# Kernel optimization log

Measured on AMD Instinct MI355X. Metric: run time of the kernel, lower is better.

The kernel has to match this reference:

```python
import jax, jax.numpy as jnp
import numpy as np

B, T, D, K = 16, 4096, 512, 128
ALPHA_MIN = 1e-06
OMEGA_MAX = float(np.pi)
SN_EPS = 1e-06


def setup_inputs() -> dict:
    key = jax.random.key(0)
    ks = jax.random.split(key, 7)
    x = jax.random.normal(ks[0], (B, T, D), jnp.float32)
    # irregular positive step sizes, mean ~ 1/T like the uniform-grid default
    dt = jax.random.uniform(ks[1], (B, T), jnp.float32, minval=0.1, maxval=1.9) * (1.0 / T)
    # replicate reset_parameters: target_alpha ~ U(0.01, 0.2), raw = log(expm1(alpha - alpha_min))
    target_alpha = jax.random.uniform(ks[2], (K,), jnp.float32, minval=0.01, maxval=0.2)
    s_real_raw = jnp.log(jnp.expm1(jnp.maximum(target_alpha - ALPHA_MIN, 1e-08)))
    s_imag = jax.random.uniform(ks[3], (K,), jnp.float32, minval=-np.pi, maxval=np.pi)
    # kaiming-uniform-ish proj weight [K, D] and bias [K]
    W = jax.random.normal(ks[4], (K, D), jnp.float32) * (1.0 / np.sqrt(D))
    bound = 1.0 / np.sqrt(D)
    bias = jax.random.uniform(ks[5], (K,), jnp.float32, minval=-bound, maxval=bound)
    b_log = jnp.zeros((K,), jnp.float32)  # torch stores [1,1,K]; broadcasting is identical
    u_sn = jax.random.normal(ks[6], (K,), jnp.float32)  # spectral-norm power-iteration vector
    return {"x": x, "dt": dt, "s_real_raw": s_real_raw, "s_imag": s_imag,
            "W": W, "bias": bias, "b_log": b_log, "u_sn": u_sn}


def _spectral_normalize(W, u):
    # one power iteration, u/v detached (as torch.nn.utils.spectral_norm does)
    v = W.T @ u
    v = v / (jnp.linalg.norm(v) + SN_EPS)
    u2 = W @ v
    u2 = u2 / (jnp.linalg.norm(u2) + SN_EPS)
    u2 = jax.lax.stop_gradient(u2)
    v = jax.lax.stop_gradient(v)
    sigma = u2 @ (W @ v)
    return W / sigma


def reference(x, dt, s_real_raw, s_imag, W, bias, b_log, u_sn):
    # x: [B,T,D], dt: [B,T] -> lap_feats [B,T,2K]
    alpha = jax.nn.softplus(s_real_raw) + ALPHA_MIN          # [K] strictly positive decay
    omega = jnp.clip(s_imag, -OMEGA_MAX, OMEGA_MAX)          # [K]
    Wsn = _spectral_normalize(W, u_sn)
    u = jnp.einsum('btd,kd->btk', x, Wsn) + bias             # spectral-norm projection
    dt3 = dt[..., None]                                      # [B,T,1]
    rho = jnp.exp(-alpha * dt3)                              # [B,T,K]
    theta = omega * dt3
    cos_t, sin_t = jnp.cos(theta), jnp.sin(theta)
    b_gain = jnp.exp(b_log)                                  # [K]
    inj = (1.0 - rho) * (b_gain * u)                         # [B,T,K]

    def step(carry, inp):
        c, s = carry
        r, ct, st, it = inp
        c_new = r * (c * ct - s * st) + it
        s_new = r * (c * st + s * ct) + it
        return (c_new, s_new), (c_new, s_new)

    seq = (jnp.moveaxis(rho, 1, 0), jnp.moveaxis(cos_t, 1, 0),
           jnp.moveaxis(sin_t, 1, 0), jnp.moveaxis(inj, 1, 0))  # each [T,B,K]
    init = (jnp.zeros((x.shape[0], K), x.dtype), jnp.zeros((x.shape[0], K), x.dtype))
    _, (C, S) = jax.lax.scan(step, init, seq)
    C = jnp.moveaxis(C, 0, 1)  # [B,T,K]
    S = jnp.moveaxis(S, 0, 1)
    return jnp.concatenate([C, S], axis=-1)
```

## Files before the change

### kernel.cpp

```cpp
#include <hip/hip_runtime.h>
#include <stdint.h>

#define BB 16
#define TT 4096
#define DDIM 512
#define KK 128
#define TCB 128
#define NCB (TT / TCB)
#define PI_F 3.14159265358979323846f

typedef unsigned short u16;
typedef __attribute__((ext_vector_type(8))) short short8;
typedef __attribute__((ext_vector_type(4))) float f32x4;

__device__ __forceinline__ uint32_t cvt_bf16_rn(float f) {
  uint32_t u = __float_as_uint(f);
  return (u + 0x7FFFu + ((u >> 16) & 1u)) >> 16;
}
__device__ __forceinline__ uint32_t pack2(float a, float b) {
  return cvt_bf16_rn(a) | (cvt_bf16_rn(b) << 16);
}
__device__ __forceinline__ void gload_lds16(const void* g, void* l) {
  __builtin_amdgcn_global_load_lds(
      (const __attribute__((address_space(1))) void*)g,
      (__attribute__((address_space(3))) void*)l, 16, 0, 0);
}

__global__ __launch_bounds__(256) void k_prep(
    const float* __restrict__ W, const float* __restrict__ u_sn,
    const float* __restrict__ s_real_raw, const float* __restrict__ s_imag,
    const float* __restrict__ bias, const float* __restrict__ b_log,
    const float* __restrict__ dt,
    float* __restrict__ params, u16* __restrict__ Wp, float* __restrict__ ct) {
  int gb = blockIdx.x;
  int tid = threadIdx.x;
  if (gb < 64) {
    int idx = gb * 256 + tid;
    int k = idx >> 7;
    int d = (idx & 127) * 4;
    float4 v = *(const float4*)&W[(size_t)k * DDIM + d];
    int tile = d >> 6, dl = d & 63;
    int slot = (dl >> 3) ^ (k & 7);
    int e = dl & 7;
    size_t base = (size_t)tile * 8192 + k * 64 + slot * 8 + e;
    uint2 p;
    p.x = pack2(v.x, v.y);
    p.y = pack2(v.z, v.w);
    *(uint2*)&Wp[base] = p;
  } else if (gb < 80) {
    __shared__ float sc[256];
    int b = gb - 64;
    const float* row = dt + (size_t)b * TT;
    float* orow = ct + (size_t)b * TT;
    float loc[16];
    float s = 0.f;
    int base = tid * 16;
    for (int i = 0; i < 16; ++i) { s += row[base + i]; loc[i] = s; }
    sc[tid] = s;
    __syncthreads();
    for (int off = 1; off < 256; off <<= 1) {
      float v = (tid >= off) ? sc[tid - off] : 0.f;
      __syncthreads();
      sc[tid] += v;
      __syncthreads();
    }
    float excl = sc[tid] - s;
    for (int i = 0; i < 16; ++i) orow[base + i] = excl + loc[i];
  } else {
    __shared__ float su[KK];
    __shared__ float sv[DDIM];
    __shared__ float red[4];
    __shared__ float wred[256];
    __shared__ float s_sig;
    if (tid < KK) su[tid] = u_sn[tid];
    __syncthreads();
    for (int rep = 0; rep < 2; ++rep) {
      int d = tid + rep * 256;
      float acc = 0.f;
      for (int k = 0; k < KK; ++k) acc += W[k * DDIM + d] * su[k];
      sv[d] = acc;
    }
    __syncthreads();
    float nn = 0.f;
    for (int rep = 0; rep < 2; ++rep) { float v = sv[tid + rep * 256]; nn += v * v; }
    for (int off = 32; off > 0; off >>= 1) nn += __shfl_down(nn, off, 64);
    if ((tid & 63) == 0) red[tid >> 6] = nn;
    __syncthreads();
    float vn2 = red[0] + red[1] + red[2] + red[3];
    __syncthreads();
    float vinv = 1.f / (sqrtf(vn2) + 1e-6f);
    for (int rep = 0; rep < 2; ++rep) sv[tid + rep * 256] *= vinv;
    __syncthreads();
    {
      int k = tid & 127, q = tid >> 7;
      const float* wrow = W + (size_t)k * DDIM + q * 256;
      float p = 0.f;
      for (int d = 0; d < 256; ++d) p += wrow[d] * sv[q * 256 + d];
      wred[tid] = p;
    }
    __syncthreads();
    float wv = 0.f;
    if (tid < KK) wv = wred[tid] + wred[tid + 128];
    float q = wv * wv;
    for (int off = 32; off > 0; off >>= 1) q += __shfl_down(q, off, 64);
    if ((tid & 63) == 0) red[tid >> 6] = q;
    __syncthreads();
    if (tid == 0) {
      float wn2 = red[0] + red[1] + red[2] + red[3];
      s_sig = wn2 / (sqrtf(wn2) + 1e-6f);
    }
    __syncthreads();
    if (tid < KK) {
      float inv_sigma = 1.f / s_sig;
      float sr = s_real_raw[tid];
      float alpha = ((sr > 20.f) ? sr : log1pf(expf(sr))) + 1e-6f;
      float om = fminf(fmaxf(s_imag[tid], -PI_F), PI_F);
      float bg = expf(b_log[tid]);
      params[tid] = alpha;
      params[KK + tid] = om;
      params[2 * KK + tid] = bg * inv_sigma;
      params[3 * KK + tid] = bg * bias[tid];
    }
  }
}

__global__ __launch_bounds__(512, 4) void k_gemm(
    const float* __restrict__ x, const u16* __restrict__ Wp,
    const float* __restrict__ dt, const float* __restrict__ ct,
    const float* __restrict__ params, u16* __restrict__ itvb,
    float* __restrict__ csum_re, float* __restrict__ csum_im) {
  __shared__ __align__(16) u16 smem[32768];

  const int chunk = blockIdx.x, b = blockIdx.y;
  const int tid = threadIdx.x;
  const int wv = tid >> 6, l = tid & 63;
  const int lm = l & 15, lg = l >> 4;
  const int kw = wv & 1, tw = wv >> 1;
  const int t0 = chunk * TCB;

  const int xr0 = tid >> 4;
  const int xc = (tid & 15) * 4;
  const size_t xbase = ((size_t)b * TT + t0 + xr0) * DDIM + xc;
  int xso[4];
#pragma unroll
  for (int q = 0; q < 4; ++q) {
    int row = xr0 + 32 * q;
    xso[q] = row * 64 + (((xc >> 3) ^ (row & 7)) << 3) + ((xc >> 2) & 1) * 4;
  }

  f32x4 acc[2][4];
#pragma unroll
  for (int m = 0; m < 2; ++m)
#pragma unroll
    for (int n = 0; n < 4; ++n) acc[m][n] = (f32x4)(0.0f);

  {
    const char* wsg = (const char*)Wp + (size_t)tid * 16;
    char* wd = (char*)smem + 32768 + tid * 16;
    gload_lds16(wsg, wd);
    gload_lds16(wsg + 8192, wd + 8192);
#pragma unroll
    for (int q = 0; q < 4; ++q) {
      float4 v = *(const float4*)(x + xbase + (size_t)(32 * q) * DDIM);
      uint2 p;
      p.x = pack2(v.x, v.y);
      p.y = pack2(v.z, v.w);
      *(uint2*)&smem[xso[q]] = p;
    }
  }
  __syncthreads();

  int cur = 0;
  for (int it = 0; it < 8; ++it) {
    float4 xf[4];
    if (it < 7) {
      const float* xp = x + xbase + (it + 1) * 64;
#pragma unroll
      for (int q = 0; q < 4; ++q)
        xf[q] = *(const float4*)(xp + (size_t)(32 * q) * DDIM);
      const char* wsg = (const char*)Wp + (size_t)(it + 1) * 16384 + tid * 16;
      char* wd = (char*)smem + 32768 + (cur ^ 1) * 16384 + tid * 16;
      gload_lds16(wsg, wd);
      gload_lds16(wsg + 8192, wd + 8192);
    }
    __builtin_amdgcn_sched_barrier(0);
    {
      const u16* xb = smem + cur * 8192;
      const u16* wb = smem + 16384 + cur * 8192;
      __builtin_amdgcn_s_setprio(1);
#pragma unroll
      for (int ks = 0; ks < 2; ++ks) {
        short8 fa[2], fb[4];
#pragma unroll
        for (int m = 0; m < 2; ++m) {
          int row = tw * 32 + m * 16 + lm;
          int sw = ((ks * 4 + lg) ^ (row & 7)) * 8;
          fa[m] = *(const short8*)&xb[row * 64 + sw];
        }
#pragma unroll
        for (int n = 0; n < 4; ++n) {
          int row = kw * 64 + n * 16 + lm;
          int sw = ((ks * 4 + lg) ^ (row & 7)) * 8;
          fb[n] = *(const short8*)&wb[row * 64 + sw];
        }
#pragma unroll
        for (int m = 0; m < 2; ++m)
#pragma unroll
          for (int n = 0; n < 4; ++n)
            acc[m][n] = __builtin_amdgcn_mfma_f32_16x16x32_bf16(fa[m], fb[n], acc[m][n], 0, 0, 0);
      }
      __builtin_amdgcn_s_setprio(0);
    }
    __builtin_amdgcn_sched_barrier(0);
    if (it < 7) {
      u16* xb = smem + (cur ^ 1) * 8192;
#pragma unroll
      for (int q = 0; q < 4; ++q) {
        uint2 p;
        p.x = pack2(xf[q].x, xf[q].y);
        p.y = pack2(xf[q].z, xf[q].w);
        *(uint2*)&xb[xso[q]] = p;
      }
    }
    __syncthreads();
    cur ^= 1;
  }

  float* totr = (float*)smem;
  float* toti = (float*)smem + 512;
  u16* litv = smem + 8192;

  float dtv[2][4], ctv[2][4];
#pragma unroll
  for (int m = 0; m < 2; ++m)
#pragma unroll
    for (int r = 0; r < 4; ++r) {
      int t = t0 + tw * 32 + m * 16 + lg * 4 + r;
      dtv[m][r] = dt[(size_t)b * TT + t];
      ctv[m][r] = ct[(size_t)b * TT + t];
    }

#pragma unroll
  for (int n = 0; n < 4; ++n) {
    int k = kw * 64 + n * 16 + lm;
    float pal = params[k], pom = params[KK + k];
    float pc1 = params[2 * KK + k], pc2 = params[3 * KK + k];
    float sr = 0.f, si2 = 0.f;
#pragma unroll
    for (int m = 0; m < 2; ++m)
#pragma unroll
      for (int r = 0; r < 4; ++r) {
        float g = acc[m][n][r];
        float a = pal * dtv[m][r];
        float omr = a * (1.f - a * (0.5f - a * (1.f / 6.f)));
        float itv = omr * (pc1 * g + pc2);
        int tl = tw * 32 + m * 16 + lg * 4 + r;
        litv[tl * KK + k] = (u16)cvt_bf16_rn(itv);
        float e = __expf(pal * ctv[m][r]);
        float sn, cs;
        __sincosf(pom * ctv[m][r], &sn, &cs);
        sr += itv * e * cs;
        si2 -= itv * e * sn;
      }
    sr += __shfl_xor(sr, 16, 64);
    sr += __shfl_xor(sr, 32, 64);
    si2 += __shfl_xor(si2, 16, 64);
    si2 += __shfl_xor(si2, 32, 64);
    if (lg == 0) { totr[tw * KK + k] = sr; toti[tw * KK + k] = si2; }
  }
  __syncthreads();

  if (tid < 256) {
    int v = tid & 127;
    float* src = (tid < 128) ? totr : toti;
    float* dst = (tid < 128) ? csum_re : csum_im;
    dst[((size_t)b * NCB + chunk) * KK + v] =
        (src[v] + src[KK + v]) + (src[2 * KK + v] + src[3 * KK + v]);
  }
  {
    int row = tid >> 4;
    int c8 = (tid & 15) * 8;
#pragma unroll
    for (int rr = 0; rr < 4; ++rr) {
      int tr = rr * 32 + row;
      uint4 v = *(const uint4*)&litv[tr * KK + c8];
      *(uint4*)&itvb[((size_t)b * TT + t0 + tr) * KK + c8] = v;
    }
  }
}

__global__ __launch_bounds__(512) void k_final(
    const u16* __restrict__ itvb, const float* __restrict__ ct,
    const float* __restrict__ params,
    const float* __restrict__ csum_re, const float* __restrict__ csum_im,
    float* __restrict__ out) {
  __shared__ float prer[KK], prei[KK];
  __shared__ float segr[16][KK], segi[16][KK];
  const int chunk = blockIdx.x, b = blockIdx.y;
  const int tid = threadIdx.x;
  const int k4 = (tid & 31) * 4, tseg = tid >> 5;
  const int tbase = chunk * TCB + tseg * 8;

  if (tid < 256) {
    int v = tid & 127;
    const float* srcp = (tid < 128) ? csum_re : csum_im;
    float* dstp = (tid < 128) ? prer : prei;
    size_t base = (size_t)b * NCB * KK + v;
    float a0 = 0.f, a1 = 0.f, a2 = 0.f, a3 = 0.f;
    int c = 0;
    for (; c + 4 <= chunk; c += 4) {
      a0 += srcp[base + (size_t)(c + 0) * KK];
      a1 += srcp[base + (size_t)(c + 1) * KK];
      a2 += srcp[base + (size_t)(c + 2) * KK];
      a3 += srcp[base + (size_t)(c + 3) * KK];
    }
    for (; c < chunk; ++c) a0 += srcp[base + (size_t)c * KK];
    dstp[v] = (a0 + a1) + (a2 + a3);
  }

  float4 pal4 = *(const float4*)&params[k4];
  float4 pom4 = *(const float4*)&params[KK + k4];
  float pal[4] = {pal4.x, pal4.y, pal4.z, pal4.w};
  float pom[4] = {pom4.x, pom4.y, pom4.z, pom4.w};

  uint2 iv8[8];
  float fr[8][4], fi[8][4];
  float sr[4] = {0.f, 0.f, 0.f, 0.f}, si[4] = {0.f, 0.f, 0.f, 0.f};
#pragma unroll
  for (int i = 0; i < 8; ++i) {
    int t = tbase + i;
    float ctv = ct[(size_t)b * TT + t];
    iv8[i] = *(const uint2*)&itvb[((size_t)b * TT + t) * KK + k4];
    float it[4] = {__uint_as_float(iv8[i].x << 16), __uint_as_float(iv8[i].x & 0xFFFF0000u),
                   __uint_as_float(iv8[i].y << 16), __uint_as_float(iv8[i].y & 0xFFFF0000u)};
#pragma unroll
    for (int c = 0; c < 4; ++c) {
      float e = __expf(pal[c] * ctv);
      float sn, cs;
      __sincosf(pom[c] * ctv, &sn, &cs);
      fr[i][c] = e * cs;
      fi[i][c] = e * sn;
      sr[c] += it[c] * fr[i][c];
      si[c] -= it[c] * fi[i][c];
    }
  }
  *(float4*)&segr[tseg][k4] = make_float4(sr[0], sr[1], sr[2], sr[3]);
  *(float4*)&segi[tseg][k4] = make_float4(si[0], si[1], si[2], si[3]);
  __syncthreads();
  float cr[4], ci[4];
  {
    float4 p0 = *(const float4*)&prer[k4];
    float4 p1 = *(const float4*)&prei[k4];
    cr[0] = p0.x; cr[1] = p0.y; cr[2] = p0.z; cr[3] = p0.w;
    ci[0] = p1.x; ci[1] = p1.y; ci[2] = p1.z; ci[3] = p1.w;
  }
  for (int s = 0; s < tseg; ++s) {
    float4 a = *(const float4*)&segr[s][k4];
    float4 bb = *(const float4*)&segi[s][k4];
    cr[0] += a.x; cr[1] += a.y; cr[2] += a.z; cr[3] += a.w;
    ci[0] += bb.x; ci[1] += bb.y; ci[2] += bb.z; ci[3] += bb.w;
  }
#pragma unroll
  for (int i = 0; i < 8; ++i) {
    int t = tbase + i;
    float it[4] = {__uint_as_float(iv8[i].x << 16), __uint_as_float(iv8[i].x & 0xFFFF0000u),
                   __uint_as_float(iv8[i].y << 16), __uint_as_float(iv8[i].y & 0xFFFF0000u)};
    float C4[4], S4[4];
#pragma unroll
    for (int c = 0; c < 4; ++c) {
      float f_r = fr[i][c], f_i = fi[i][c];
      cr[c] += it[c] * f_r;
      ci[c] -= it[c] * f_i;
      float inv = __builtin_amdgcn_rcpf(f_r * f_r + f_i * f_i);
      float Rw = (cr[c] * f_r - ci[c] * f_i) * inv;
      float Iw = (cr[c] * f_i + ci[c] * f_r) * inv;
      C4[c] = Rw - Iw;
      S4[c] = Rw + Iw;
    }
    size_t rowb = ((size_t)b * TT + t) * (2 * KK);
    *(float4*)&out[rowb + k4] = make_float4(C4[0], C4[1], C4[2], C4[3]);
    *(float4*)&out[rowb + KK + k4] = make_float4(S4[0], S4[1], S4[2], S4[3]);
  }
}

extern "C" void kernel_launch(void* const* d_in, const int* in_sizes, int n_in,
                              void* d_out, int out_size, void* d_ws, size_t ws_size,
                              hipStream_t stream) {
  const float* x    = (const float*)d_in[0];
  const float* dt   = (const float*)d_in[1];
  const float* srr  = (const float*)d_in[2];
  const float* si   = (const float*)d_in[3];
  const float* W    = (const float*)d_in[4];
  const float* bias = (const float*)d_in[5];
  const float* blog = (const float*)d_in[6];
  const float* usn  = (const float*)d_in[7];
  float* out = (float*)d_out;
  float* ws = (float*)d_ws;

  float* params  = ws;
  float* ct      = ws + 4 * KK;
  float* csum_re = ct + (size_t)BB * TT;
  float* csum_im = csum_re + (size_t)BB * NCB * KK;
  u16*   Wp      = (u16*)(csum_im + (size_t)BB * NCB * KK);
  u16*   itvb    = Wp + 65536;

  k_prep<<<81, 256, 0, stream>>>(W, usn, srr, si, bias, blog, dt, params, Wp, ct);
  k_gemm<<<dim3(NCB, BB), 512, 0, stream>>>(x, Wp, dt, ct, params, itvb,
                                            csum_re, csum_im);
  k_final<<<dim3(NCB, BB), 512, 0, stream>>>(itvb, ct, params,
                                             csum_re, csum_im, out);
}
```

Before: 67.44 us.

## Halve GEMM time-chunk to 64 rows with single-buffered W for higher occupancy

The projection kernel now handles 64-timestep chunks instead of 128, with 8 waves split 4-way over K and 2-way over time. Shared memory drops to 32KB by single-buffering the W tile and double-buffering only x, and launch bounds request 8 blocks per CU. The final scan kernel keeps 128-step chunks and sums twice as many partial chunk sums for its prefix. This launches more, smaller blocks to raise occupancy and parallelism. In exchange it adds an extra barrier per K-step, explicit waitcnts that serialize the W load, and redundant W traffic across more blocks.

Result: slower. 70.55 us (+4.6%).

```diff
diff --git a/kernel.cpp b/kernel.cpp
--- a/kernel.cpp
+++ b/kernel.cpp
@@ -5,8 +5,10 @@
 #define TT 4096
 #define DDIM 512
 #define KK 128
-#define TCB 128
-#define NCB (TT / TCB)
+#define TCA 64
+#define NCA (TT / TCA)
+#define TCF 128
+#define NCF (TT / TCF)
 #define PI_F 3.14159265358979323846f
 
 typedef unsigned short u16;
@@ -124,73 +126,68 @@
   }
 }
 
-__global__ __launch_bounds__(512, 4) void k_gemm(
+__global__ __launch_bounds__(512, 8) void k_gemm(
     const float* __restrict__ x, const u16* __restrict__ Wp,
     const float* __restrict__ dt, const float* __restrict__ ct,
     const float* __restrict__ params, u16* __restrict__ itvb,
     float* __restrict__ csum_re, float* __restrict__ csum_im) {
-  __shared__ __align__(16) u16 smem[32768];
-
-  const int chunk = blockIdx.x, b = blockIdx.y;
+  __shared__ __align__(16) u16 smem[16384];
+
+  const int ca = blockIdx.x, b = blockIdx.y;
   const int tid = threadIdx.x;
   const int wv = tid >> 6, l = tid & 63;
   const int lm = l & 15, lg = l >> 4;
-  const int kw = wv & 1, tw = wv >> 1;
-  const int t0 = chunk * TCB;
-
-  const int xr0 = tid >> 4;
-  const int xc = (tid & 15) * 4;
-  const size_t xbase = ((size_t)b * TT + t0 + xr0) * DDIM + xc;
-  int xso[4];
-#pragma unroll
-  for (int q = 0; q < 4; ++q) {
-    int row = xr0 + 32 * q;
-    xso[q] = row * 64 + (((xc >> 3) ^ (row & 7)) << 3) + ((xc >> 2) & 1) * 4;
-  }
-
-  f32x4 acc[2][4];
+  const int kw = wv & 3, tw = wv >> 2;
+  const int t0 = ca * TCA;
+
+  const int xr = tid >> 3, xc8 = tid & 7;
+  const size_t xbase = ((size_t)b * TT + t0 + xr) * DDIM + xc8 * 8;
+  const int xsoff = xr * 64 + ((xc8 ^ (xr & 7)) << 3);
+
+  const char* wsrc = (const char*)Wp + (size_t)tid * 16;
+  char* wdst = (char*)smem + 16384 + tid * 16;
+
+  f32x4 acc[2][2];
 #pragma unroll
   for (int m = 0; m < 2; ++m)
 #pragma unroll
-    for (int n = 0; n < 4; ++n) acc[m][n] = (f32x4)(0.0f);
+    for (int n = 0; n < 2; ++n) acc[m][n] = (f32x4)(0.0f);
 
   {
-    const char* wsg = (const char*)Wp + (size_t)tid * 16;
-    char* wd = (char*)smem + 32768 + tid * 16;
-    gload_lds16(wsg, wd);
-    gload_lds16(wsg + 8192, wd + 8192);
-#pragma unroll
-    for (int q = 0; q < 4; ++q) {
-      float4 v = *(const float4*)(x + xbase + (size_t)(32 * q) * DDIM);
-      uint2 p;
-      p.x = pack2(v.x, v.y);
-      p.y = pack2(v.z, v.w);
-      *(uint2*)&smem[xso[q]] = p;
-    }
-  }
-  __syncthreads();
-
-  int cur = 0;
-  for (int it = 0; it < 8; ++it) {
-    float4 xf[4];
-    if (it < 7) {
-      const float* xp = x + xbase + (it + 1) * 64;
-#pragma unroll
-      for (int q = 0; q < 4; ++q)
-        xf[q] = *(const float4*)(xp + (size_t)(32 * q) * DDIM);
-      const char* wsg = (const char*)Wp + (size_t)(it + 1) * 16384 + tid * 16;
-      char* wd = (char*)smem + 32768 + (cur ^ 1) * 16384 + tid * 16;
-      gload_lds16(wsg, wd);
-      gload_lds16(wsg + 8192, wd + 8192);
+    gload_lds16(wsrc, wdst);
+    gload_lds16(wsrc + 8192, wdst + 8192);
+    float4 f0 = *(const float4*)(x + xbase);
+    float4 f1 = *(const float4*)(x + xbase + 4);
+    __builtin_amdgcn_sched_barrier(0);
+    asm volatile("s_waitcnt vmcnt(0)" ::: "memory");
+    uint4 p;
+    p.x = pack2(f0.x, f0.y);
+    p.y = pack2(f0.z, f0.w);
+    p.z = pack2(f1.x, f1.y);
+    p.w = pack2(f1.z, f1.w);
+    *(uint4*)&smem[xsoff] = p;
+    asm volatile("s_waitcnt lgkmcnt(0)" ::: "memory");
+    __builtin_amdgcn_s_barrier();
+    __builtin_amdgcn_sched_barrier(0);
+  }
+
+  int p = 0;
+#pragma unroll
+  for (int j = 0; j < 8; ++j) {
+    float4 xf0, xf1;
+    if (j < 7) {
+      const float* xp = x + xbase + (j + 1) * 64;
+      xf0 = *(const float4*)(xp);
+      xf1 = *(const float4*)(xp + 4);
     }
     __builtin_amdgcn_sched_barrier(0);
     {
-      const u16* xb = smem + cur * 8192;
-      const u16* wb = smem + 16384 + cur * 8192;
+      const u16* xb = smem + p * 4096;
+      const u16* wb = smem + 8192;
       __builtin_amdgcn_s_setprio(1);
 #pragma unroll
       for (int ks = 0; ks < 2; ++ks) {
-        short8 fa[2], fb[4];
+        short8 fa[2], fb[2];
 #pragma unroll
         for (int m = 0; m < 2; ++m) {
           int row = tw * 32 + m * 16 + lm;
@@ -198,37 +195,45 @@
           fa[m] = *(const short8*)&xb[row * 64 + sw];
         }
 #pragma unroll
-        for (int n = 0; n < 4; ++n) {
-          int row = kw * 64 + n * 16 + lm;
+        for (int n = 0; n < 2; ++n) {
+          int row = kw * 32 + n * 16 + lm;
           int sw = ((ks * 4 + lg) ^ (row & 7)) * 8;
           fb[n] = *(const short8*)&wb[row * 64 + sw];
         }
 #pragma unroll
         for (int m = 0; m < 2; ++m)
 #pragma unroll
-          for (int n = 0; n < 4; ++n)
+          for (int n = 0; n < 2; ++n)
             acc[m][n] = __builtin_amdgcn_mfma_f32_16x16x32_bf16(fa[m], fb[n], acc[m][n], 0, 0, 0);
       }
       __builtin_amdgcn_s_setprio(0);
     }
     __builtin_amdgcn_sched_barrier(0);
-    if (it < 7) {
-      u16* xb = smem + (cur ^ 1) * 8192;
-#pragma unroll
-      for (int q = 0; q < 4; ++q) {
-        uint2 p;
-        p.x = pack2(xf[q].x, xf[q].y);
-        p.y = pack2(xf[q].z, xf[q].w);
-        *(uint2*)&xb[xso[q]] = p;
-      }
-    }
-    __syncthreads();
-    cur ^= 1;
-  }
-
-  float* totr = (float*)smem;
-  float* toti = (float*)smem + 512;
-  u16* litv = smem + 8192;
+    if (j < 7) {
+      __builtin_amdgcn_s_barrier();
+      __builtin_amdgcn_sched_barrier(0);
+      const char* wsg = (const char*)Wp + (size_t)(j + 1) * 16384 + tid * 16;
+      gload_lds16(wsg, wdst);
+      gload_lds16(wsg + 8192, wdst + 8192);
+      __builtin_amdgcn_sched_barrier(0);
+      asm volatile("s_waitcnt vmcnt(0)" ::: "memory");
+      uint4 pk;
+      pk.x = pack2(xf0.x, xf0.y);
+      pk.y = pack2(xf0.z, xf0.w);
+      pk.z = pack2(xf1.x, xf1.y);
+      pk.w = pack2(xf1.z, xf1.w);
+      *(uint4*)&smem[(p ^ 1) * 4096 + xsoff] = pk;
+      asm volatile("s_waitcnt lgkmcnt(0)" ::: "memory");
+      __builtin_amdgcn_s_barrier();
+      __builtin_amdgcn_sched_barrier(0);
+      p ^= 1;
+    }
+  }
+  __syncthreads();
+
+  u16* litv = smem;
+  float* totr = (float*)(smem + 8192);
+  float* toti = totr + 256;
 
   float dtv[2][4], ctv[2][4];
 #pragma unroll
@@ -241,8 +246,8 @@
     }
 
 #pragma unroll
-  for (int n = 0; n < 4; ++n) {
-    int k = kw * 64 + n * 16 + lm;
+  for (int n = 0; n < 2; ++n) {
+    int k = kw * 32 + n * 16 + lm;
     float pal = params[k], pom = params[KK + k];
     float pc1 = params[2 * KK + k], pc2 = params[3 * KK + k];
     float sr = 0.f, si2 = 0.f;
@@ -274,14 +279,13 @@
     int v = tid & 127;
     float* src = (tid < 128) ? totr : toti;
     float* dst = (tid < 128) ? csum_re : csum_im;
-    dst[((size_t)b * NCB + chunk) * KK + v] =
-        (src[v] + src[KK + v]) + (src[2 * KK + v] + src[3 * KK + v]);
+    dst[((size_t)b * NCA + ca) * KK + v] = src[v] + src[KK + v];
   }
   {
     int row = tid >> 4;
     int c8 = (tid & 15) * 8;
 #pragma unroll
-    for (int rr = 0; rr < 4; ++rr) {
+    for (int rr = 0; rr < 2; ++rr) {
       int tr = rr * 32 + row;
       uint4 v = *(const uint4*)&litv[tr * KK + c8];
       *(uint4*)&itvb[((size_t)b * TT + t0 + tr) * KK + c8] = v;
@@ -299,22 +303,23 @@
   const int chunk = blockIdx.x, b = blockIdx.y;
   const int tid = threadIdx.x;
   const int k4 = (tid & 31) * 4, tseg = tid >> 5;
-  const int tbase = chunk * TCB + tseg * 8;
+  const int tbase = chunk * TCF + tseg * 8;
 
   if (tid < 256) {
     int v = tid & 127;
     const float* srcp = (tid < 128) ? csum_re : csum_im;
     float* dstp = (tid < 128) ? prer : prei;
-    size_t base = (size_t)b * NCB * KK + v;
+    size_t base = (size_t)b * NCA * KK + v;
+    int lim = 2 * chunk;
     float a0 = 0.f, a1 = 0.f, a2 = 0.f, a3 = 0.f;
     int c = 0;
-    for (; c + 4 <= chunk; c += 4) {
+    for (; c + 4 <= lim; c += 4) {
       a0 += srcp[base + (size_t)(c + 0) * KK];
       a1 += srcp[base + (size_t)(c + 1) * KK];
       a2 += srcp[base + (size_t)(c + 2) * KK];
       a3 += srcp[base + (size_t)(c + 3) * KK];
     }
-    for (; c < chunk; ++c) a0 += srcp[base + (size_t)c * KK];
+    for (; c < lim; ++c) a0 += srcp[base + (size_t)c * KK];
     dstp[v] = (a0 + a1) + (a2 + a3);
   }
 
@@ -400,13 +405,13 @@
   float* params  = ws;
   float* ct      = ws + 4 * KK;
   float* csum_re = ct + (size_t)BB * TT;
-  float* csum_im = csum_re + (size_t)BB * NCB * KK;
-  u16*   Wp      = (u16*)(csum_im + (size_t)BB * NCB * KK);
+  float* csum_im = csum_re + (size_t)BB * NCA * KK;
+  u16*   Wp      = (u16*)(csum_im + (size_t)BB * NCA * KK);
   u16*   itvb    = Wp + 65536;
 
   k_prep<<<81, 256, 0, stream>>>(W, usn, srr, si, bias, blog, dt, params, Wp, ct);
-  k_gemm<<<dim3(NCB, BB), 512, 0, stream>>>(x, Wp, dt, ct, params, itvb,
+  k_gemm<<<dim3(NCA, BB), 512, 0, stream>>>(x, Wp, dt, ct, params, itvb,
                                             csum_re, csum_im);
-  k_final<<<dim3(NCB, BB), 512, 0, stream>>>(itvb, ct, params,
+  k_final<<<dim3(NCF, BB), 512, 0, stream>>>(itvb, ct, params,
                                              csum_re, csum_im, out);
 }
```
